# Kernel tuning notes

Hardware: AMD Instinct MI355X
Metric: run time of the kernel (lower is better)

## Reference

```python
import jax, jax.numpy as jnp
import numpy as np

DIM = 32
ED = DIM * DIM          # 1024
HID = ED * 4            # 4096
EPS = 1e-5


def _ln(x, g, b):
    # LayerNorm over last two dims (d, d)
    m = x.mean(axis=(-2, -1), keepdims=True)
    v = jnp.var(x, axis=(-2, -1), keepdims=True)
    return (x - m) * jax.lax.rsqrt(v + EPS) * g + b


def setup_inputs() -> dict:
    key = jax.random.key(0)
    ks = jax.random.split(key, 10)
    b, s, d = 2, 1024, DIM
    inp = {
        "x": jax.random.normal(ks[0], (b, s, d, d), dtype=jnp.float32),
        # StateSpaceLayer params
        "log_A": jax.random.normal(ks[1], (d,), dtype=jnp.float32) * 0.02,
        "w_dt": jax.random.normal(ks[2], (d,), dtype=jnp.float32) / np.sqrt(d),
        "b_dt": jnp.zeros((), dtype=jnp.float32),
        "g_ssm": jnp.ones((d, d), dtype=jnp.float32),
        "b_ssm": jnp.zeros((d, d), dtype=jnp.float32),
        # FFN params
        "g_ffn": jnp.ones((d, d), dtype=jnp.float32),
        "b_ffn": jnp.zeros((d, d), dtype=jnp.float32),
        "W1": jax.random.normal(ks[3], (ED, HID), dtype=jnp.float32) / np.sqrt(ED),
        "bb1": jnp.zeros((HID,), dtype=jnp.float32),
        "W2": jax.random.normal(ks[4], (HID, ED), dtype=jnp.float32) / np.sqrt(HID),
        "bb2": jnp.zeros((ED,), dtype=jnp.float32),
    }
    return inp


def reference(x, log_A, w_dt, b_dt, g_ssm, b_ssm, g_ffn, b_ffn, W1, bb1, W2, bb2):
    b, s, d, _ = x.shape
    # ---- StateSpaceLayer (parallel / training path) ----
    xn = _ln(x, g_ssm, b_ssm)                          # (b,s,d,d)
    A_cont = -jnp.exp(log_A)                           # (d,)
    # dt_proj: Linear(d,1) over last axis, then squeeze -> (b,s,d)
    dt = jax.nn.softplus(jnp.einsum('bsrc,c->bsr', xn, w_dt) + b_dt)
    log_a = dt * A_cont                                # (b,s,d)
    cs = jnp.cumsum(log_a, axis=1)                     # (b,s,d)
    log_M = cs[:, :, None, :] - cs[:, None, :, :]      # (b,t,j,d)
    tmask = jnp.arange(s)[:, None] >= jnp.arange(s)[None, :]  # (t,j) causal
    M = jnp.where(tmask[None, :, :, None], jnp.exp(log_M), 0.0)
    ssm_out = jnp.einsum('btjr,bjrc->btrc', M, xn) + x  # residual
    # ---- MatrixFeedForward ----
    fn = _ln(ssm_out, g_ffn, b_ffn).reshape(b, s, d * d)
    h = jax.nn.gelu(fn @ W1 + bb1, approximate=False)
    y = (h @ W2 + bb2).reshape(b, s, d, d)
    return ssm_out + y
```

## Files before the change

### kernel.cpp

```cpp
#include <hip/hip_runtime.h>
#include <math.h>

#define EPSF 1e-5f

typedef __attribute__((ext_vector_type(4))) float f32x4;
typedef __attribute__((ext_vector_type(2))) long long2v;

__device__ __forceinline__ unsigned short f2bf(float f) {
  unsigned int u = __float_as_uint(f);
  u += 0x7FFFu + ((u >> 16) & 1u);
  return (unsigned short)(u >> 16);
}
__device__ __forceinline__ float bf2f(unsigned short u) {
  return __uint_as_float((unsigned int)u << 16);
}


__global__ __launch_bounds__(256) void k_pre(
    const float* __restrict__ x, const float* __restrict__ g, const float* __restrict__ bta,
    const float* __restrict__ w_dt, const float* __restrict__ b_dt,
    const float* __restrict__ log_A, unsigned short* __restrict__ xn, float* __restrict__ log_a,
    const float* __restrict__ W1, unsigned char* __restrict__ W1t,
    const float* __restrict__ W2, unsigned char* __restrict__ W2t) {
  __shared__ float smem[64 * 65];
  int tid = threadIdx.x;
  if (blockIdx.x < 2048) {
    int bs = blockIdx.x;
    int t = tid;
    float4 v = ((const float4*)(x + (size_t)bs * 1024))[t];
    float s = v.x + v.y + v.z + v.w;
    float ss = v.x * v.x + v.y * v.y + v.z * v.z + v.w * v.w;
    #pragma unroll
    for (int o = 1; o < 64; o <<= 1) { s += __shfl_xor(s, o); ss += __shfl_xor(ss, o); }
    float* red = smem;
    int w = t >> 6;
    if ((t & 63) == 0) { red[w] = s; red[4 + w] = ss; }
    __syncthreads();
    float S = red[0] + red[1] + red[2] + red[3];
    float SS = red[4] + red[5] + red[6] + red[7];
    float m = S * (1.0f / 1024.0f);
    float var = SS * (1.0f / 1024.0f) - m * m;
    float inv = rsqrtf(var + EPSF);
    float4 gv = ((const float4*)g)[t];
    float4 bv = ((const float4*)bta)[t];
    float4 o;
    o.x = (v.x - m) * inv * gv.x + bv.x;
    o.y = (v.y - m) * inv * gv.y + bv.y;
    o.z = (v.z - m) * inv * gv.z + bv.z;
    o.w = (v.w - m) * inv * gv.w + bv.w;
    ushort4 ob;
    ob.x = f2bf(o.x); ob.y = f2bf(o.y); ob.z = f2bf(o.z); ob.w = f2bf(o.w);
    ((ushort4*)(xn + (size_t)bs * 1024))[t] = ob;
    float4 wv = ((const float4*)w_dt)[t & 7];
    float part = o.x * wv.x + o.y * wv.y + o.z * wv.z + o.w * wv.w;
    part += __shfl_xor(part, 1);
    part += __shfl_xor(part, 2);
    part += __shfl_xor(part, 4);
    if ((t & 7) == 0) {
      int r = t >> 3;
      float z = part + b_dt[0];
      float sp = (z > 20.0f) ? z : log1pf(expf(z));
      log_a[(size_t)bs * 32 + r] = sp * (-expf(log_A[r]));
    }
  } else {
    int bid = blockIdx.x - 2048;
    bool isW1 = bid < 1024;
    const float* src; unsigned char* dst; int C, r0, c0, nkgp;
    if (isW1) { src = W1; dst = W1t; C = 4096; nkgp = 16;
                c0 = (bid & 63) * 64; r0 = (bid >> 6) * 64; }
    else { bid -= 1024; src = W2; dst = W2t; C = 1024; nkgp = 64;
           c0 = (bid & 15) * 64; r0 = (bid >> 4) * 64; }
    #pragma unroll
    for (int q = 0; q < 4; ++q) {
      int lin = q * 256 + tid;
      int r = lin >> 4, cq = lin & 15;
      float4 v = *(const float4*)(src + (size_t)(r0 + r) * C + c0 + cq * 4);
      smem[r * 65 + cq * 4 + 0] = v.x; smem[r * 65 + cq * 4 + 1] = v.y;
      smem[r * 65 + cq * 4 + 2] = v.z; smem[r * 65 + cq * 4 + 3] = v.w;
    }
    __syncthreads();
    #pragma unroll
    for (int q = 0; q < 2; ++q) {
      int lin = q * 256 + tid;
      int c = lin & 63, rh = lin >> 6;
      int n = c0 + c, k = r0 + rh * 8;
      int nt = n >> 4, l15n = n & 15;
      int kp = k >> 6, qd = (k >> 3) & 3, half = (k >> 5) & 1;
      int p0 = __builtin_amdgcn_cvt_pk_fp8_f32(
          smem[(rh * 8 + 0) * 65 + c] * 16.0f, smem[(rh * 8 + 1) * 65 + c] * 16.0f, 0, false);
      p0 = __builtin_amdgcn_cvt_pk_fp8_f32(
          smem[(rh * 8 + 2) * 65 + c] * 16.0f, smem[(rh * 8 + 3) * 65 + c] * 16.0f, p0, true);
      int p1 = __builtin_amdgcn_cvt_pk_fp8_f32(
          smem[(rh * 8 + 4) * 65 + c] * 16.0f, smem[(rh * 8 + 5) * 65 + c] * 16.0f, 0, false);
      p1 = __builtin_amdgcn_cvt_pk_fp8_f32(
          smem[(rh * 8 + 6) * 65 + c] * 16.0f, smem[(rh * 8 + 7) * 65 + c] * 16.0f, p1, true);
      int2 pk; pk.x = p0; pk.y = p1;
      *(int2*)(dst + ((size_t)(nt * nkgp + kp)) * 1024 + (qd * 16 + l15n) * 16 + half * 8) = pk;
    }
  }
}

template <int PASS>
__global__ __launch_bounds__(256) void k_scan_pass(
    const unsigned short* __restrict__ xn, const float* __restrict__ x,
    const float* __restrict__ loga, float4* __restrict__ E, float* __restrict__ P,
    const float* __restrict__ bb2, float* __restrict__ out) {
  int bx = blockIdx.x;
  int b = bx >> 8, r = (bx >> 3) & 31, ch = bx & 7;
  int tid = threadIdx.x, cg = tid & 7, sub = tid >> 3;
  __shared__ float dec[128];
  __shared__ float4 sE[32][8];
  __shared__ float sP[32];
  if (tid < 128)
    dec[tid] = expf(loga[(size_t)(b * 1024 + ch * 128 + tid) * 32 + r]);
  __syncthreads();
  int t0 = ch * 128 + sub * 4;
  size_t base = ((size_t)(b * 1024 + t0) * 1024 + r * 32 + cg * 4) >> 2;
  const ushort4* xn4 = (const ushort4*)xn;
  float4 xv[4];
  #pragma unroll
  for (int i = 0; i < 4; ++i) {
    ushort4 u = xn4[base + (size_t)i * 256];
    xv[i].x = bf2f(u.x); xv[i].y = bf2f(u.y); xv[i].z = bf2f(u.z); xv[i].w = bf2f(u.w);
  }
  float4 S = {0.f, 0.f, 0.f, 0.f};
  float Pl = 1.0f;
  #pragma unroll
  for (int i = 0; i < 4; ++i) {
    float d = dec[sub * 4 + i];
    S.x = d * S.x + xv[i].x; S.y = d * S.y + xv[i].y;
    S.z = d * S.z + xv[i].z; S.w = d * S.w + xv[i].w;
    Pl *= d;
  }
  sE[sub][cg] = S;
  if (cg == 0) sP[sub] = Pl;
  __syncthreads();
  if (PASS == 0) {
    if (tid < 8) {
      float4 Et = {0.f, 0.f, 0.f, 0.f};
      float PP = 1.0f;
      #pragma unroll
      for (int h = 0; h < 32; ++h) {
        float p = sP[h]; float4 e = sE[h][tid];
        Et.x = p * Et.x + e.x; Et.y = p * Et.y + e.y;
        Et.z = p * Et.z + e.z; Et.w = p * Et.w + e.w;
        PP *= p;
      }
      E[((size_t)(b * 32 + r) * 8 + ch) * 8 + tid] = Et;
      if (tid == 0) P[(b * 32 + r) * 8 + ch] = PP;
    }
  } else {
    float4 Sin = {0.f, 0.f, 0.f, 0.f};
    const float4* Eb = E + (size_t)(b * 32 + r) * 64 + cg;
    const float* Pb = P + (size_t)(b * 32 + r) * 8;
    for (int h = 0; h < ch; ++h) {
      float p = Pb[h]; float4 e = Eb[h * 8];
      Sin.x = p * Sin.x + e.x; Sin.y = p * Sin.y + e.y;
      Sin.z = p * Sin.z + e.z; Sin.w = p * Sin.w + e.w;
    }
    for (int h = 0; h < sub; ++h) {
      float p = sP[h]; float4 e = sE[h][cg];
      Sin.x = p * Sin.x + e.x; Sin.y = p * Sin.y + e.y;
      Sin.z = p * Sin.z + e.z; Sin.w = p * Sin.w + e.w;
    }
    float4 bb = ((const float4*)bb2)[r * 8 + cg];
    const float4* x4 = (const float4*)x;
    float4* out4 = (float4*)out;
    #pragma unroll
    for (int i = 0; i < 4; ++i) {
      float d = dec[sub * 4 + i];
      Sin.x = d * Sin.x + xv[i].x; Sin.y = d * Sin.y + xv[i].y;
      Sin.z = d * Sin.z + xv[i].z; Sin.w = d * Sin.w + xv[i].w;
      float4 rx = x4[base + (size_t)i * 256];
      float4 oi;
      oi.x = Sin.x + rx.x + bb.x; oi.y = Sin.y + rx.y + bb.y;
      oi.z = Sin.z + rx.z + bb.z; oi.w = Sin.w + rx.w + bb.w;
      out4[base + (size_t)i * 256] = oi;
    }
  }
}

__global__ __launch_bounds__(256) void k_ln2(
    const float* __restrict__ out, const float* __restrict__ bb2,
    const float* __restrict__ g, const float* __restrict__ bta,
    unsigned char* __restrict__ fn) {
  int bs = blockIdx.x;
  int t = threadIdx.x;
  float4 v = ((const float4*)(out + (size_t)bs * 1024))[t];
  float4 bb = ((const float4*)bb2)[t];
  v.x -= bb.x; v.y -= bb.y; v.z -= bb.z; v.w -= bb.w;
  float s = v.x + v.y + v.z + v.w;
  float ss = v.x * v.x + v.y * v.y + v.z * v.z + v.w * v.w;
  #pragma unroll
  for (int o = 1; o < 64; o <<= 1) { s += __shfl_xor(s, o); ss += __shfl_xor(ss, o); }
  __shared__ float red[8];
  int w = t >> 6;
  if ((t & 63) == 0) { red[w] = s; red[4 + w] = ss; }
  __syncthreads();
  float S = red[0] + red[1] + red[2] + red[3];
  float SS = red[4] + red[5] + red[6] + red[7];
  float m = S * (1.0f / 1024.0f);
  float var = SS * (1.0f / 1024.0f) - m * m;
  float inv = rsqrtf(var + EPSF);
  float4 gv = ((const float4*)g)[t];
  float4 bv = ((const float4*)bta)[t];
  float f0 = (v.x - m) * inv * gv.x + bv.x;
  float f1 = (v.y - m) * inv * gv.y + bv.y;
  float f2 = (v.z - m) * inv * gv.z + bv.z;
  float f3 = (v.w - m) * inv * gv.w + bv.w;
  int p = __builtin_amdgcn_cvt_pk_fp8_f32(f0, f1, 0, false);
  p = __builtin_amdgcn_cvt_pk_fp8_f32(f2, f3, p, true);
  int mt = bs >> 4, l15m = bs & 15;
  int kp = t >> 4, qd = (t >> 1) & 3, half = (t >> 3) & 1, j0 = (t & 1) * 4;
  *(int*)(fn + ((size_t)(mt * 16 + kp)) * 1024 + (qd * 16 + l15m) * 16 + half * 8 + j0) = p;
}

__global__ __launch_bounds__(256, 2) void k_gemm1(
    const unsigned char* __restrict__ Ap, const unsigned char* __restrict__ Bp,
    const float* __restrict__ bias, unsigned char* __restrict__ C8) {
  constexpr int NKGP = 16, ITERP = 16;
  __shared__ __align__(16) unsigned char sC[16384];
  int L = blockIdx.x;
  int xcd = L & 7;
  int nq = xcd & 3, mh = xcd >> 2;
  int rest = L >> 3;
  int nx = rest & 7, my = rest >> 3;
  int n0 = (nq * 8 + nx) * 128;
  int m0 = (mh * 8 + my) * 128;
  int tid = threadIdx.x;
  int wave = tid >> 6, lane = tid & 63;
  int wr = wave >> 1, wc = wave & 1;
  int l15 = lane & 15, quad = lane >> 4;
  int mt0 = (m0 >> 4) + wr * 4;
  int nt0 = (n0 >> 4) + wc * 4;
  const unsigned char* pa = Ap + (size_t)mt0 * NKGP * 1024 + lane * 16;
  const unsigned char* pb = Bp + (size_t)nt0 * NKGP * 1024 + lane * 16;

  f32x4 zero = {0.0f, 0.0f, 0.0f, 0.0f};
  f32x4 acc[4][4];
  #pragma unroll
  for (int i = 0; i < 4; ++i)
    #pragma unroll
    for (int j = 0; j < 4; ++j) acc[i][j] = zero;

  long2v a[4][4], b[4][4];
  #pragma unroll
  for (int s = 0; s < 4; ++s)
    #pragma unroll
    for (int i = 0; i < 4; ++i) {
      a[s][i] = *(const long2v*)(pa + ((size_t)i * NKGP + s) * 1024);
      b[s][i] = *(const long2v*)(pb + ((size_t)i * NKGP + s) * 1024);
    }
  #pragma unroll 1
  for (int kp = 0; kp < ITERP - 4; kp += 4) {
    #pragma unroll
    for (int s = 0; s < 4; ++s) {
      #pragma unroll
      for (int i = 0; i < 4; ++i)
        #pragma unroll
        for (int j = 0; j < 4; ++j)
          acc[i][j] = __builtin_amdgcn_mfma_f32_16x16x32_fp8_fp8(a[s][i].x, b[s][j].x, acc[i][j], 0, 0, 0);
      #pragma unroll
      for (int i = 0; i < 4; ++i)
        #pragma unroll
        for (int j = 0; j < 4; ++j)
          acc[i][j] = __builtin_amdgcn_mfma_f32_16x16x32_fp8_fp8(a[s][i].y, b[s][j].y, acc[i][j], 0, 0, 0);
      #pragma unroll
      for (int i = 0; i < 4; ++i) {
        a[s][i] = *(const long2v*)(pa + ((size_t)i * NKGP + kp + 4 + s) * 1024);
        b[s][i] = *(const long2v*)(pb + ((size_t)i * NKGP + kp + 4 + s) * 1024);
      }
    }
  }
  #pragma unroll
  for (int s = 0; s < 4; ++s) {
    #pragma unroll
    for (int i = 0; i < 4; ++i)
      #pragma unroll
      for (int j = 0; j < 4; ++j)
        acc[i][j] = __builtin_amdgcn_mfma_f32_16x16x32_fp8_fp8(a[s][i].x, b[s][j].x, acc[i][j], 0, 0, 0);
    #pragma unroll
    for (int i = 0; i < 4; ++i)
      #pragma unroll
      for (int j = 0; j < 4; ++j)
        acc[i][j] = __builtin_amdgcn_mfma_f32_16x16x32_fp8_fp8(a[s][i].y, b[s][j].y, acc[i][j], 0, 0, 0);
  }

  #pragma unroll
  for (int i = 0; i < 4; ++i) {
    #pragma unroll
    for (int j = 0; j < 4; ++j) {
      int col_l = wc * 64 + j * 16 + l15;
      float bval = bias[n0 + col_l];
      int kp_l = col_l >> 6, q2 = (col_l >> 3) & 3, half2 = (col_l >> 5) & 1, j2 = col_l & 7;
      unsigned char* ldst = sC + ((wr * 4 + i) * 2 + kp_l) * 1024 + q2 * 256 + half2 * 8 + j2;
      float vv[4];
      #pragma unroll
      for (int v = 0; v < 4; ++v) {
        float val = acc[i][j][v] * 0.0625f + bval;
        vv[v] = 0.5f * val * (1.0f + erff(val * 0.70710678118654752f));
      }
      int p01 = __builtin_amdgcn_cvt_pk_fp8_f32(vv[0], vv[1], 0, false);
      int p23 = __builtin_amdgcn_cvt_pk_fp8_f32(vv[2], vv[3], 0, false);
      ldst[(quad * 4 + 0) * 16] = (unsigned char)(p01 & 0xff);
      ldst[(quad * 4 + 1) * 16] = (unsigned char)((p01 >> 8) & 0xff);
      ldst[(quad * 4 + 2) * 16] = (unsigned char)(p23 & 0xff);
      ldst[(quad * 4 + 3) * 16] = (unsigned char)((p23 >> 8) & 0xff);
    }
  }
  __syncthreads();
  int mt2_0 = m0 >> 4, kp2_0 = n0 >> 6;
  #pragma unroll
  for (int p = 0; p < 4; ++p) {
    int ci = p * 256 + tid;
    int sb = ci >> 6, off = (ci & 63) * 16;
    int mt2 = mt2_0 + (sb >> 1), kp2 = kp2_0 + (sb & 1);
    *(int4*)(C8 + ((size_t)(mt2 * 64 + kp2)) * 1024 + off) =
        *(const int4*)(sC + sb * 1024 + off);
  }
}

__global__ __launch_bounds__(256, 2) void k_gemm2(
    const unsigned char* __restrict__ Ap, const unsigned char* __restrict__ Bp,
    float* __restrict__ O) {
  constexpr int NKGP = 64, ITERP = 16;
  int L = blockIdx.x;
  int xcd = L & 7;
  int ks = xcd >> 1, mh = xcd & 1;
  int rest = L >> 3;
  int nx = rest & 7, my = rest >> 3;
  int n0 = nx * 128;
  int m0 = (mh * 8 + my) * 128;
  int kp0 = ks * ITERP;
  int tid = threadIdx.x;
  int wave = tid >> 6, lane = tid & 63;
  int wr = wave >> 1, wc = wave & 1;
  int l15 = lane & 15, quad = lane >> 4;
  int mt0 = (m0 >> 4) + wr * 4;
  int nt0 = (n0 >> 4) + wc * 4;
  const unsigned char* pa = Ap + ((size_t)mt0 * NKGP + kp0) * 1024 + lane * 16;
  const unsigned char* pb = Bp + ((size_t)nt0 * NKGP + kp0) * 1024 + lane * 16;

  f32x4 zero = {0.0f, 0.0f, 0.0f, 0.0f};
  f32x4 acc[4][4];
  #pragma unroll
  for (int i = 0; i < 4; ++i)
    #pragma unroll
    for (int j = 0; j < 4; ++j) acc[i][j] = zero;

  long2v a[4][4], b[4][4];
  #pragma unroll
  for (int s = 0; s < 4; ++s)
    #pragma unroll
    for (int i = 0; i < 4; ++i) {
      a[s][i] = *(const long2v*)(pa + ((size_t)i * NKGP + s) * 1024);
      b[s][i] = *(const long2v*)(pb + ((size_t)i * NKGP + s) * 1024);
    }
  #pragma unroll 1
  for (int kp = 0; kp < ITERP - 4; kp += 4) {
    #pragma unroll
    for (int s = 0; s < 4; ++s) {
      #pragma unroll
      for (int i = 0; i < 4; ++i)
        #pragma unroll
        for (int j = 0; j < 4; ++j)
          acc[i][j] = __builtin_amdgcn_mfma_f32_16x16x32_fp8_fp8(a[s][i].x, b[s][j].x, acc[i][j], 0, 0, 0);
      #pragma unroll
      for (int i = 0; i < 4; ++i)
        #pragma unroll
        for (int j = 0; j < 4; ++j)
          acc[i][j] = __builtin_amdgcn_mfma_f32_16x16x32_fp8_fp8(a[s][i].y, b[s][j].y, acc[i][j], 0, 0, 0);
      #pragma unroll
      for (int i = 0; i < 4; ++i) {
        a[s][i] = *(const long2v*)(pa + ((size_t)i * NKGP + kp + 4 + s) * 1024);
        b[s][i] = *(const long2v*)(pb + ((size_t)i * NKGP + kp + 4 + s) * 1024);
      }
    }
  }
  #pragma unroll
  for (int s = 0; s < 4; ++s) {
    #pragma unroll
    for (int i = 0; i < 4; ++i)
      #pragma unroll
      for (int j = 0; j < 4; ++j)
        acc[i][j] = __builtin_amdgcn_mfma_f32_16x16x32_fp8_fp8(a[s][i].x, b[s][j].x, acc[i][j], 0, 0, 0);
    #pragma unroll
    for (int i = 0; i < 4; ++i)
      #pragma unroll
      for (int j = 0; j < 4; ++j)
        acc[i][j] = __builtin_amdgcn_mfma_f32_16x16x32_fp8_fp8(a[s][i].y, b[s][j].y, acc[i][j], 0, 0, 0);
  }

  #pragma unroll
  for (int i = 0; i < 4; ++i)
    #pragma unroll
    for (int j = 0; j < 4; ++j) {
      int col = n0 + wc * 64 + j * 16 + l15;
      #pragma unroll
      for (int v = 0; v < 4; ++v) {
        int row = m0 + wr * 64 + i * 16 + quad * 4 + v;
        atomicAdd(&O[(size_t)row * 1024 + col], acc[i][j][v] * 0.0625f);
      }
    }
}

extern "C" void kernel_launch(void* const* d_in, const int* in_sizes, int n_in,
                              void* d_out, int out_size, void* d_ws, size_t ws_size,
                              hipStream_t stream) {
  const float* x     = (const float*)d_in[0];
  const float* log_A = (const float*)d_in[1];
  const float* w_dt  = (const float*)d_in[2];
  const float* b_dt  = (const float*)d_in[3];
  const float* g_ssm = (const float*)d_in[4];
  const float* b_ssm = (const float*)d_in[5];
  const float* g_ffn = (const float*)d_in[6];
  const float* b_ffn = (const float*)d_in[7];
  const float* W1    = (const float*)d_in[8];
  const float* bb1   = (const float*)d_in[9];
  const float* W2    = (const float*)d_in[10];
  const float* bb2   = (const float*)d_in[11];
  float* out = (float*)d_out;

  const size_t MB = 1u << 20;
  char* ws = (char*)d_ws;
  unsigned short* xn   = (unsigned short*)(ws);
  unsigned char* W1t   = (unsigned char*)(ws + 4 * MB);
  float* loga          = (float*)(ws + 8 * MB);
  float4* Ebuf         = (float4*)(ws + 8 * MB + 262144);
  float* Pbuf          = (float*)(ws + 8 * MB + 393216);
  unsigned char* fn    = (unsigned char*)(ws + 9 * MB);
  unsigned char* W2t   = (unsigned char*)(ws + 11 * MB);
  unsigned char* hbf   = (unsigned char*)(ws + 15 * MB);

  k_pre<<<4096, 256, 0, stream>>>(x, g_ssm, b_ssm, w_dt, b_dt, log_A, xn, loga,
                                  W1, W1t, W2, W2t);
  k_scan_pass<0><<<512, 256, 0, stream>>>(xn, x, loga, Ebuf, Pbuf, bb2, out);
  k_scan_pass<1><<<512, 256, 0, stream>>>(xn, x, loga, Ebuf, Pbuf, bb2, out);
  k_ln2<<<2048, 256, 0, stream>>>(out, bb2, g_ffn, b_ffn, fn);
  k_gemm1<<<512, 256, 0, stream>>>(fn, W1t, bb1, hbf);
  k_gemm2<<<512, 256, 0, stream>>>(hbf, W2t, out);
}
```

Before: 174.6 us.

## Stage GEMM operand tiles in LDS via async global-to-LDS loads

The two FP8 GEMM kernels are merged into one template that stages A and B tiles in a 64KB shared buffer. Each wave issues global_load_lds copies for its share of the tiles, and every wave then reads its fragments from LDS. Before, each wave fetched its own fragments straight from global memory into registers. The goal is to share operand loads across waves and cut redundant global traffic and register pressure. In exchange the pipeline is single-buffered, with two barriers per stage and no overlap of load and compute, and 64KB of LDS per block may limit occupancy.

After: 173.9 us. No clear change (-0.4%).

```diff
diff --git a/kernel.cpp b/kernel.cpp
--- a/kernel.cpp
+++ b/kernel.cpp
@@ -13,6 +13,12 @@
 }
 __device__ __forceinline__ float bf2f(unsigned short u) {
   return __uint_as_float((unsigned int)u << 16);
+}
+
+__device__ __forceinline__ void async_load16(const void* g, void* l) {
+  __builtin_amdgcn_global_load_lds(
+      (const __attribute__((address_space(1))) void*)g,
+      (__attribute__((address_space(3))) void*)l, 16, 0, 0);
 }
 
 
@@ -215,26 +221,37 @@
   *(int*)(fn + ((size_t)(mt * 16 + kp)) * 1024 + (qd * 16 + l15m) * 16 + half * 8 + j0) = p;
 }
 
-__global__ __launch_bounds__(256, 2) void k_gemm1(
+template <int EPI, int NKGP>
+__global__ __launch_bounds__(256, 2) void k_gemm_lds(
     const unsigned char* __restrict__ Ap, const unsigned char* __restrict__ Bp,
-    const float* __restrict__ bias, unsigned char* __restrict__ C8) {
-  constexpr int NKGP = 16, ITERP = 16;
-  __shared__ __align__(16) unsigned char sC[16384];
+    const float* __restrict__ bias, void* __restrict__ C) {
+  __shared__ __align__(16) unsigned char sAB[65536];
+  unsigned char* sA = sAB;
+  unsigned char* sB = sAB + 32768;
   int L = blockIdx.x;
-  int xcd = L & 7;
-  int nq = xcd & 3, mh = xcd >> 2;
-  int rest = L >> 3;
-  int nx = rest & 7, my = rest >> 3;
-  int n0 = (nq * 8 + nx) * 128;
-  int m0 = (mh * 8 + my) * 128;
+  int m0, n0, kp0;
+  if (EPI == 0) {
+    int xcd = L & 7;
+    int nq = xcd & 3, mh = xcd >> 2;
+    int rest = L >> 3;
+    int nx = rest & 7, my = rest >> 3;
+    n0 = (nq * 8 + nx) * 128;
+    m0 = (mh * 8 + my) * 128;
+    kp0 = 0;
+  } else {
+    int xcd = L & 7;
+    int ks = xcd >> 1, mh = xcd & 1;
+    int rest = L >> 3;
+    int nx = rest & 7, my = rest >> 3;
+    n0 = nx * 128;
+    m0 = (mh * 8 + my) * 128;
+    kp0 = ks * 16;
+  }
   int tid = threadIdx.x;
   int wave = tid >> 6, lane = tid & 63;
   int wr = wave >> 1, wc = wave & 1;
   int l15 = lane & 15, quad = lane >> 4;
-  int mt0 = (m0 >> 4) + wr * 4;
-  int nt0 = (n0 >> 4) + wc * 4;
-  const unsigned char* pa = Ap + (size_t)mt0 * NKGP * 1024 + lane * 16;
-  const unsigned char* pb = Bp + (size_t)nt0 * NKGP * 1024 + lane * 16;
+  int mt0b = m0 >> 4, nt0b = n0 >> 4;
 
   f32x4 zero = {0.0f, 0.0f, 0.0f, 0.0f};
   f32x4 acc[4][4];
@@ -243,165 +260,94 @@
     #pragma unroll
     for (int j = 0; j < 4; ++j) acc[i][j] = zero;
 
-  long2v a[4][4], b[4][4];
-  #pragma unroll
-  for (int s = 0; s < 4; ++s)
-    #pragma unroll
-    for (int i = 0; i < 4; ++i) {
-      a[s][i] = *(const long2v*)(pa + ((size_t)i * NKGP + s) * 1024);
-      b[s][i] = *(const long2v*)(pb + ((size_t)i * NKGP + s) * 1024);
-    }
+  const unsigned char* gsrc = (wave < 2) ? Ap : Bp;
+  int rt0 = (wave < 2) ? mt0b : nt0b;
+  unsigned char* ldst = ((wave < 2) ? sA : sB) + (wave & 1) * 16384;
+  int sb0 = (wave & 1) * 16;
+
   #pragma unroll 1
-  for (int kp = 0; kp < ITERP - 4; kp += 4) {
-    #pragma unroll
-    for (int s = 0; s < 4; ++s) {
+  for (int st = 0; st < 4; ++st) {
+    int kps = kp0 + st * 4;
+    #pragma unroll
+    for (int t = 0; t < 16; ++t) {
+      int sb = sb0 + t;
+      int rt = sb >> 2, kl = sb & 3;
+      async_load16(gsrc + ((size_t)(rt0 + rt) * NKGP + kps + kl) * 1024 + lane * 16,
+                   ldst + t * 1024);
+    }
+    __syncthreads();
+    #pragma unroll
+    for (int kl = 0; kl < 4; ++kl) {
+      long2v af[4], bf[4];
+      #pragma unroll
+      for (int i = 0; i < 4; ++i)
+        af[i] = *(const long2v*)(sA + ((wr * 4 + i) * 4 + kl) * 1024 + lane * 16);
+      #pragma unroll
+      for (int j = 0; j < 4; ++j)
+        bf[j] = *(const long2v*)(sB + ((wc * 4 + j) * 4 + kl) * 1024 + lane * 16);
       #pragma unroll
       for (int i = 0; i < 4; ++i)
         #pragma unroll
         for (int j = 0; j < 4; ++j)
-          acc[i][j] = __builtin_amdgcn_mfma_f32_16x16x32_fp8_fp8(a[s][i].x, b[s][j].x, acc[i][j], 0, 0, 0);
+          acc[i][j] = __builtin_amdgcn_mfma_f32_16x16x32_fp8_fp8(af[i].x, bf[j].x, acc[i][j], 0, 0, 0);
       #pragma unroll
       for (int i = 0; i < 4; ++i)
         #pragma unroll
         for (int j = 0; j < 4; ++j)
-          acc[i][j] = __builtin_amdgcn_mfma_f32_16x16x32_fp8_fp8(a[s][i].y, b[s][j].y, acc[i][j], 0, 0, 0);
-      #pragma unroll
-      for (int i = 0; i < 4; ++i) {
-        a[s][i] = *(const long2v*)(pa + ((size_t)i * NKGP + kp + 4 + s) * 1024);
-        b[s][i] = *(const long2v*)(pb + ((size_t)i * NKGP + kp + 4 + s) * 1024);
+          acc[i][j] = __builtin_amdgcn_mfma_f32_16x16x32_fp8_fp8(af[i].y, bf[j].y, acc[i][j], 0, 0, 0);
+    }
+    __syncthreads();
+  }
+
+  if (EPI == 0) {
+    unsigned char* sC = sAB;
+    #pragma unroll
+    for (int i = 0; i < 4; ++i) {
+      #pragma unroll
+      for (int j = 0; j < 4; ++j) {
+        int col_l = wc * 64 + j * 16 + l15;
+        float bval = bias[n0 + col_l];
+        int kp_l = col_l >> 6, q2 = (col_l >> 3) & 3, half2 = (col_l >> 5) & 1, j2 = col_l & 7;
+        unsigned char* ld = sC + ((wr * 4 + i) * 2 + kp_l) * 1024 + q2 * 256 + half2 * 8 + j2;
+        float vv[4];
+        #pragma unroll
+        for (int v = 0; v < 4; ++v) {
+          float val = acc[i][j][v] * 0.0625f + bval;
+          vv[v] = 0.5f * val * (1.0f + erff(val * 0.70710678118654752f));
+        }
+        int p01 = __builtin_amdgcn_cvt_pk_fp8_f32(vv[0], vv[1], 0, false);
+        int p23 = __builtin_amdgcn_cvt_pk_fp8_f32(vv[2], vv[3], 0, false);
+        ld[(quad * 4 + 0) * 16] = (unsigned char)(p01 & 0xff);
+        ld[(quad * 4 + 1) * 16] = (unsigned char)((p01 >> 8) & 0xff);
+        ld[(quad * 4 + 2) * 16] = (unsigned char)(p23 & 0xff);
+        ld[(quad * 4 + 3) * 16] = (unsigned char)((p23 >> 8) & 0xff);
       }
     }
-  }
-  #pragma unroll
-  for (int s = 0; s < 4; ++s) {
+    __syncthreads();
+    unsigned char* C8 = (unsigned char*)C;
+    int mt2_0 = m0 >> 4, kp2_0 = n0 >> 6;
+    #pragma unroll
+    for (int p = 0; p < 4; ++p) {
+      int ci = p * 256 + tid;
+      int sb = ci >> 6, off = (ci & 63) * 16;
+      int mt2 = mt2_0 + (sb >> 1), kp2 = kp2_0 + (sb & 1);
+      *(int4*)(C8 + ((size_t)(mt2 * 64 + kp2)) * 1024 + off) =
+          *(const int4*)(sC + sb * 1024 + off);
+    }
+  } else {
+    float* O = (float*)C;
     #pragma unroll
     for (int i = 0; i < 4; ++i)
       #pragma unroll
-      for (int j = 0; j < 4; ++j)
-        acc[i][j] = __builtin_amdgcn_mfma_f32_16x16x32_fp8_fp8(a[s][i].x, b[s][j].x, acc[i][j], 0, 0, 0);
-    #pragma unroll
-    for (int i = 0; i < 4; ++i)
-      #pragma unroll
-      for (int j = 0; j < 4; ++j)
-        acc[i][j] = __builtin_amdgcn_mfma_f32_16x16x32_fp8_fp8(a[s][i].y, b[s][j].y, acc[i][j], 0, 0, 0);
-  }
-
-  #pragma unroll
-  for (int i = 0; i < 4; ++i) {
-    #pragma unroll
-    for (int j = 0; j < 4; ++j) {
-      int col_l = wc * 64 + j * 16 + l15;
-      float bval = bias[n0 + col_l];
-      int kp_l = col_l >> 6, q2 = (col_l >> 3) & 3, half2 = (col_l >> 5) & 1, j2 = col_l & 7;
-      unsigned char* ldst = sC + ((wr * 4 + i) * 2 + kp_l) * 1024 + q2 * 256 + half2 * 8 + j2;
-      float vv[4];
-      #pragma unroll
-      for (int v = 0; v < 4; ++v) {
-        float val = acc[i][j][v] * 0.0625f + bval;
-        vv[v] = 0.5f * val * (1.0f + erff(val * 0.70710678118654752f));
+      for (int j = 0; j < 4; ++j) {
+        int col = n0 + wc * 64 + j * 16 + l15;
+        #pragma unroll
+        for (int v = 0; v < 4; ++v) {
+          int row = m0 + wr * 64 + i * 16 + quad * 4 + v;
+          atomicAdd(&O[(size_t)row * 1024 + col], acc[i][j][v] * 0.0625f);
+        }
       }
-      int p01 = __builtin_amdgcn_cvt_pk_fp8_f32(vv[0], vv[1], 0, false);
-      int p23 = __builtin_amdgcn_cvt_pk_fp8_f32(vv[2], vv[3], 0, false);
-      ldst[(quad * 4 + 0) * 16] = (unsigned char)(p01 & 0xff);
-      ldst[(quad * 4 + 1) * 16] = (unsigned char)((p01 >> 8) & 0xff);
-      ldst[(quad * 4 + 2) * 16] = (unsigned char)(p23 & 0xff);
-      ldst[(quad * 4 + 3) * 16] = (unsigned char)((p23 >> 8) & 0xff);
-    }
-  }
-  __syncthreads();
-  int mt2_0 = m0 >> 4, kp2_0 = n0 >> 6;
-  #pragma unroll
-  for (int p = 0; p < 4; ++p) {
-    int ci = p * 256 + tid;
-    int sb = ci >> 6, off = (ci & 63) * 16;
-    int mt2 = mt2_0 + (sb >> 1), kp2 = kp2_0 + (sb & 1);
-    *(int4*)(C8 + ((size_t)(mt2 * 64 + kp2)) * 1024 + off) =
-        *(const int4*)(sC + sb * 1024 + off);
-  }
-}
-
-__global__ __launch_bounds__(256, 2) void k_gemm2(
-    const unsigned char* __restrict__ Ap, const unsigned char* __restrict__ Bp,
-    float* __restrict__ O) {
-  constexpr int NKGP = 64, ITERP = 16;
-  int L = blockIdx.x;
-  int xcd = L & 7;
-  int ks = xcd >> 1, mh = xcd & 1;
-  int rest = L >> 3;
-  int nx = rest & 7, my = rest >> 3;
-  int n0 = nx * 128;
-  int m0 = (mh * 8 + my) * 128;
-  int kp0 = ks * ITERP;
-  int tid = threadIdx.x;
-  int wave = tid >> 6, lane = tid & 63;
-  int wr = wave >> 1, wc = wave & 1;
-  int l15 = lane & 15, quad = lane >> 4;
-  int mt0 = (m0 >> 4) + wr * 4;
-  int nt0 = (n0 >> 4) + wc * 4;
-  const unsigned char* pa = Ap + ((size_t)mt0 * NKGP + kp0) * 1024 + lane * 16;
-  const unsigned char* pb = Bp + ((size_t)nt0 * NKGP + kp0) * 1024 + lane * 16;
-
-  f32x4 zero = {0.0f, 0.0f, 0.0f, 0.0f};
-  f32x4 acc[4][4];
-  #pragma unroll
-  for (int i = 0; i < 4; ++i)
-    #pragma unroll
-    for (int j = 0; j < 4; ++j) acc[i][j] = zero;
-
-  long2v a[4][4], b[4][4];
-  #pragma unroll
-  for (int s = 0; s < 4; ++s)
-    #pragma unroll
-    for (int i = 0; i < 4; ++i) {
-      a[s][i] = *(const long2v*)(pa + ((size_t)i * NKGP + s) * 1024);
-      b[s][i] = *(const long2v*)(pb + ((size_t)i * NKGP + s) * 1024);
-    }
-  #pragma unroll 1
-  for (int kp = 0; kp < ITERP - 4; kp += 4) {
-    #pragma unroll
-    for (int s = 0; s < 4; ++s) {
-      #pragma unroll
-      for (int i = 0; i < 4; ++i)
-        #pragma unroll
-        for (int j = 0; j < 4; ++j)
-          acc[i][j] = __builtin_amdgcn_mfma_f32_16x16x32_fp8_fp8(a[s][i].x, b[s][j].x, acc[i][j], 0, 0, 0);
-      #pragma unroll
-      for (int i = 0; i < 4; ++i)
-        #pragma unroll
-        for (int j = 0; j < 4; ++j)
-          acc[i][j] = __builtin_amdgcn_mfma_f32_16x16x32_fp8_fp8(a[s][i].y, b[s][j].y, acc[i][j], 0, 0, 0);
-      #pragma unroll
-      for (int i = 0; i < 4; ++i) {
-        a[s][i] = *(const long2v*)(pa + ((size_t)i * NKGP + kp + 4 + s) * 1024);
-        b[s][i] = *(const long2v*)(pb + ((size_t)i * NKGP + kp + 4 + s) * 1024);
-      }
-    }
-  }
-  #pragma unroll
-  for (int s = 0; s < 4; ++s) {
-    #pragma unroll
-    for (int i = 0; i < 4; ++i)
-      #pragma unroll
-      for (int j = 0; j < 4; ++j)
-        acc[i][j] = __builtin_amdgcn_mfma_f32_16x16x32_fp8_fp8(a[s][i].x, b[s][j].x, acc[i][j], 0, 0, 0);
-    #pragma unroll
-    for (int i = 0; i < 4; ++i)
-      #pragma unroll
-      for (int j = 0; j < 4; ++j)
-        acc[i][j] = __builtin_amdgcn_mfma_f32_16x16x32_fp8_fp8(a[s][i].y, b[s][j].y, acc[i][j], 0, 0, 0);
-  }
-
-  #pragma unroll
-  for (int i = 0; i < 4; ++i)
-    #pragma unroll
-    for (int j = 0; j < 4; ++j) {
-      int col = n0 + wc * 64 + j * 16 + l15;
-      #pragma unroll
-      for (int v = 0; v < 4; ++v) {
-        int row = m0 + wr * 64 + i * 16 + quad * 4 + v;
-        atomicAdd(&O[(size_t)row * 1024 + col], acc[i][j][v] * 0.0625f);
-      }
-    }
+  }
 }
 
 extern "C" void kernel_launch(void* const* d_in, const int* in_sizes, int n_in,
@@ -437,6 +383,6 @@
   k_scan_pass<0><<<512, 256, 0, stream>>>(xn, x, loga, Ebuf, Pbuf, bb2, out);
   k_scan_pass<1><<<512, 256, 0, stream>>>(xn, x, loga, Ebuf, Pbuf, bb2, out);
   k_ln2<<<2048, 256, 0, stream>>>(out, bb2, g_ffn, b_ffn, fn);
-  k_gemm1<<<512, 256, 0, stream>>>(fn, W1t, bb1, hbf);
-  k_gemm2<<<512, 256, 0, stream>>>(hbf, W2t, out);
-}
+  k_gemm_lds<0, 16><<<512, 256, 0, stream>>>(fn, W1t, bb1, (void*)hbf);
+  k_gemm_lds<1, 64><<<512, 256, 0, stream>>>(hbf, W2t, nullptr, (void*)out);
+}
```

## Fuse all phases into one cooperative persistent kernel with grid syncs

Applied to the files above, without the earlier changes.

Turns the six separate kernels into device phase functions and runs them in a single cooperative launch of 512 blocks, with grid-wide syncs and thread fences between phases. Each block loops over several units in the pre and LayerNorm phases. The aim is to remove the launch gaps and tail idle time between kernels. In exchange, grid syncs add barrier cost and the occupancy is fixed at two blocks per CU with a shared dynamic smem size. If the cooperative launch fails, the code falls back to the per-phase kernels.

After: 185.9 us. 6.5% more time.

```diff
diff --git a/kernel.cpp b/kernel.cpp
--- a/kernel.cpp
+++ b/kernel.cpp
@@ -1,7 +1,11 @@
 #include <hip/hip_runtime.h>
+#include <hip/hip_cooperative_groups.h>
 #include <math.h>
 
+namespace cg = cooperative_groups;
+
 #define EPSF 1e-5f
+#define SMEM_BYTES 16640
 
 typedef __attribute__((ext_vector_type(4))) float f32x4;
 typedef __attribute__((ext_vector_type(2))) long long2v;
@@ -16,16 +20,18 @@
 }
 
 
-__global__ __launch_bounds__(256) void k_pre(
+
+__device__ void phase_pre(int unit, char* smem_raw,
     const float* __restrict__ x, const float* __restrict__ g, const float* __restrict__ bta,
     const float* __restrict__ w_dt, const float* __restrict__ b_dt,
     const float* __restrict__ log_A, unsigned short* __restrict__ xn, float* __restrict__ log_a,
     const float* __restrict__ W1, unsigned char* __restrict__ W1t,
     const float* __restrict__ W2, unsigned char* __restrict__ W2t) {
-  __shared__ float smem[64 * 65];
+  float* smem = (float*)smem_raw;
   int tid = threadIdx.x;
-  if (blockIdx.x < 2048) {
-    int bs = blockIdx.x;
+  __syncthreads();
+  if (unit < 2048) {
+    int bs = unit;
     int t = tid;
     float4 v = ((const float4*)(x + (size_t)bs * 1024))[t];
     float s = v.x + v.y + v.z + v.w;
@@ -63,7 +69,7 @@
       log_a[(size_t)bs * 32 + r] = sp * (-expf(log_A[r]));
     }
   } else {
-    int bid = blockIdx.x - 2048;
+    int bid = unit - 2048;
     bool isW1 = bid < 1024;
     const float* src; unsigned char* dst; int C, r0, c0, nkgp;
     if (isW1) { src = W1; dst = W1t; C = 4096; nkgp = 16;
@@ -101,21 +107,21 @@
 }
 
 template <int PASS>
-__global__ __launch_bounds__(256) void k_scan_pass(
+__device__ void phase_scan(int bx, char* smem_raw,
     const unsigned short* __restrict__ xn, const float* __restrict__ x,
     const float* __restrict__ loga, float4* __restrict__ E, float* __restrict__ P,
     const float* __restrict__ bb2, float* __restrict__ out) {
-  int bx = blockIdx.x;
+  float4* sE = (float4*)smem_raw;
+  float* dec = (float*)(smem_raw + 4096);
+  float* sP  = (float*)(smem_raw + 4608);
   int b = bx >> 8, r = (bx >> 3) & 31, ch = bx & 7;
-  int tid = threadIdx.x, cg = tid & 7, sub = tid >> 3;
-  __shared__ float dec[128];
-  __shared__ float4 sE[32][8];
-  __shared__ float sP[32];
+  int tid = threadIdx.x, cg_ = tid & 7, sub = tid >> 3;
+  __syncthreads();
   if (tid < 128)
     dec[tid] = expf(loga[(size_t)(b * 1024 + ch * 128 + tid) * 32 + r]);
   __syncthreads();
   int t0 = ch * 128 + sub * 4;
-  size_t base = ((size_t)(b * 1024 + t0) * 1024 + r * 32 + cg * 4) >> 2;
+  size_t base = ((size_t)(b * 1024 + t0) * 1024 + r * 32 + cg_ * 4) >> 2;
   const ushort4* xn4 = (const ushort4*)xn;
   float4 xv[4];
   #pragma unroll
@@ -132,8 +138,8 @@
     S.z = d * S.z + xv[i].z; S.w = d * S.w + xv[i].w;
     Pl *= d;
   }
-  sE[sub][cg] = S;
-  if (cg == 0) sP[sub] = Pl;
+  sE[sub * 8 + cg_] = S;
+  if (cg_ == 0) sP[sub] = Pl;
   __syncthreads();
   if (PASS == 0) {
     if (tid < 8) {
@@ -141,7 +147,7 @@
       float PP = 1.0f;
       #pragma unroll
       for (int h = 0; h < 32; ++h) {
-        float p = sP[h]; float4 e = sE[h][tid];
+        float p = sP[h]; float4 e = sE[h * 8 + tid];
         Et.x = p * Et.x + e.x; Et.y = p * Et.y + e.y;
         Et.z = p * Et.z + e.z; Et.w = p * Et.w + e.w;
         PP *= p;
@@ -151,7 +157,7 @@
     }
   } else {
     float4 Sin = {0.f, 0.f, 0.f, 0.f};
-    const float4* Eb = E + (size_t)(b * 32 + r) * 64 + cg;
+    const float4* Eb = E + (size_t)(b * 32 + r) * 64 + cg_;
     const float* Pb = P + (size_t)(b * 32 + r) * 8;
     for (int h = 0; h < ch; ++h) {
       float p = Pb[h]; float4 e = Eb[h * 8];
@@ -159,11 +165,11 @@
       Sin.z = p * Sin.z + e.z; Sin.w = p * Sin.w + e.w;
     }
     for (int h = 0; h < sub; ++h) {
-      float p = sP[h]; float4 e = sE[h][cg];
+      float p = sP[h]; float4 e = sE[h * 8 + cg_];
       Sin.x = p * Sin.x + e.x; Sin.y = p * Sin.y + e.y;
       Sin.z = p * Sin.z + e.z; Sin.w = p * Sin.w + e.w;
     }
-    float4 bb = ((const float4*)bb2)[r * 8 + cg];
+    float4 bb = ((const float4*)bb2)[r * 8 + cg_];
     const float4* x4 = (const float4*)x;
     float4* out4 = (float4*)out;
     #pragma unroll
@@ -180,12 +186,13 @@
   }
 }
 
-__global__ __launch_bounds__(256) void k_ln2(
+__device__ void phase_ln2(int bs, char* smem_raw,
     const float* __restrict__ out, const float* __restrict__ bb2,
     const float* __restrict__ g, const float* __restrict__ bta,
     unsigned char* __restrict__ fn) {
-  int bs = blockIdx.x;
+  float* red = (float*)smem_raw;
   int t = threadIdx.x;
+  __syncthreads();
   float4 v = ((const float4*)(out + (size_t)bs * 1024))[t];
   float4 bb = ((const float4*)bb2)[t];
   v.x -= bb.x; v.y -= bb.y; v.z -= bb.z; v.w -= bb.w;
@@ -193,7 +200,6 @@
   float ss = v.x * v.x + v.y * v.y + v.z * v.z + v.w * v.w;
   #pragma unroll
   for (int o = 1; o < 64; o <<= 1) { s += __shfl_xor(s, o); ss += __shfl_xor(ss, o); }
-  __shared__ float red[8];
   int w = t >> 6;
   if ((t & 63) == 0) { red[w] = s; red[4 + w] = ss; }
   __syncthreads();
@@ -215,12 +221,11 @@
   *(int*)(fn + ((size_t)(mt * 16 + kp)) * 1024 + (qd * 16 + l15m) * 16 + half * 8 + j0) = p;
 }
 
-__global__ __launch_bounds__(256, 2) void k_gemm1(
+__device__ void phase_gemm1(int L, char* smem_raw,
     const unsigned char* __restrict__ Ap, const unsigned char* __restrict__ Bp,
     const float* __restrict__ bias, unsigned char* __restrict__ C8) {
   constexpr int NKGP = 16, ITERP = 16;
-  __shared__ __align__(16) unsigned char sC[16384];
-  int L = blockIdx.x;
+  unsigned char* sC = (unsigned char*)smem_raw;
   int xcd = L & 7;
   int nq = xcd & 3, mh = xcd >> 2;
   int rest = L >> 3;
@@ -286,6 +291,7 @@
         acc[i][j] = __builtin_amdgcn_mfma_f32_16x16x32_fp8_fp8(a[s][i].y, b[s][j].y, acc[i][j], 0, 0, 0);
   }
 
+  __syncthreads();
   #pragma unroll
   for (int i = 0; i < 4; ++i) {
     #pragma unroll
@@ -293,7 +299,7 @@
       int col_l = wc * 64 + j * 16 + l15;
       float bval = bias[n0 + col_l];
       int kp_l = col_l >> 6, q2 = (col_l >> 3) & 3, half2 = (col_l >> 5) & 1, j2 = col_l & 7;
-      unsigned char* ldst = sC + ((wr * 4 + i) * 2 + kp_l) * 1024 + q2 * 256 + half2 * 8 + j2;
+      unsigned char* ld = sC + ((wr * 4 + i) * 2 + kp_l) * 1024 + q2 * 256 + half2 * 8 + j2;
       float vv[4];
       #pragma unroll
       for (int v = 0; v < 4; ++v) {
@@ -302,10 +308,10 @@
       }
       int p01 = __builtin_amdgcn_cvt_pk_fp8_f32(vv[0], vv[1], 0, false);
       int p23 = __builtin_amdgcn_cvt_pk_fp8_f32(vv[2], vv[3], 0, false);
-      ldst[(quad * 4 + 0) * 16] = (unsigned char)(p01 & 0xff);
-      ldst[(quad * 4 + 1) * 16] = (unsigned char)((p01 >> 8) & 0xff);
-      ldst[(quad * 4 + 2) * 16] = (unsigned char)(p23 & 0xff);
-      ldst[(quad * 4 + 3) * 16] = (unsigned char)((p23 >> 8) & 0xff);
+      ld[(quad * 4 + 0) * 16] = (unsigned char)(p01 & 0xff);
+      ld[(quad * 4 + 1) * 16] = (unsigned char)((p01 >> 8) & 0xff);
+      ld[(quad * 4 + 2) * 16] = (unsigned char)(p23 & 0xff);
+      ld[(quad * 4 + 3) * 16] = (unsigned char)((p23 >> 8) & 0xff);
     }
   }
   __syncthreads();
@@ -320,11 +326,10 @@
   }
 }
 
-__global__ __launch_bounds__(256, 2) void k_gemm2(
+__device__ void phase_gemm2(int L,
     const unsigned char* __restrict__ Ap, const unsigned char* __restrict__ Bp,
     float* __restrict__ O) {
   constexpr int NKGP = 64, ITERP = 16;
-  int L = blockIdx.x;
   int xcd = L & 7;
   int ks = xcd >> 1, mh = xcd & 1;
   int rest = L >> 3;
@@ -402,6 +407,50 @@
         atomicAdd(&O[(size_t)row * 1024 + col], acc[i][j][v] * 0.0625f);
       }
     }
+}
+
+
+#define ALL_PARAMS \
+    const float* x, const float* log_A, const float* w_dt, const float* b_dt, \
+    const float* g_ssm, const float* b_ssm, const float* g_ffn, const float* b_ffn, \
+    const float* W1, const float* bb1, const float* W2, const float* bb2, \
+    float* out, unsigned short* xn, unsigned char* W1t, float* loga, \
+    float4* Ebuf, float* Pbuf, unsigned char* fn, unsigned char* W2t, unsigned char* hbf
+
+#define ALL_ARGS x, log_A, w_dt, b_dt, g_ssm, b_ssm, g_ffn, b_ffn, W1, bb1, W2, bb2, \
+    out, xn, W1t, loga, Ebuf, Pbuf, fn, W2t, hbf
+
+__global__ __launch_bounds__(256, 2) void k_mega(ALL_PARAMS) {
+  extern __shared__ char smem[];
+  cg::grid_group gg = cg::this_grid();
+  int bid = blockIdx.x;
+  #pragma unroll 1
+  for (int u = 0; u < 8; ++u)
+    phase_pre(bid * 8 + u, smem, x, g_ssm, b_ssm, w_dt, b_dt, log_A, xn, loga, W1, W1t, W2, W2t);
+  __threadfence(); gg.sync(); __threadfence();
+  phase_scan<0>(bid, smem, xn, x, loga, Ebuf, Pbuf, bb2, out);
+  __threadfence(); gg.sync(); __threadfence();
+  phase_scan<1>(bid, smem, xn, x, loga, Ebuf, Pbuf, bb2, out);
+  __threadfence(); gg.sync(); __threadfence();
+  #pragma unroll 1
+  for (int q = 0; q < 4; ++q)
+    phase_ln2(bid * 4 + q, smem, out, bb2, g_ffn, b_ffn, fn);
+  __threadfence(); gg.sync(); __threadfence();
+  phase_gemm1(bid, smem, fn, W1t, bb1, hbf);
+  __threadfence(); gg.sync(); __threadfence();
+  phase_gemm2(bid, hbf, W2t, out);
+}
+
+template <int P>
+__global__ __launch_bounds__(256, 2) void k_phase(ALL_PARAMS) {
+  extern __shared__ char smem[];
+  int bid = blockIdx.x;
+  if (P == 0) phase_pre(bid, smem, x, g_ssm, b_ssm, w_dt, b_dt, log_A, xn, loga, W1, W1t, W2, W2t);
+  if (P == 1) phase_scan<0>(bid, smem, xn, x, loga, Ebuf, Pbuf, bb2, out);
+  if (P == 2) phase_scan<1>(bid, smem, xn, x, loga, Ebuf, Pbuf, bb2, out);
+  if (P == 3) phase_ln2(bid, smem, out, bb2, g_ffn, b_ffn, fn);
+  if (P == 4) phase_gemm1(bid, smem, fn, W1t, bb1, hbf);
+  if (P == 5) phase_gemm2(bid, hbf, W2t, out);
 }
 
 extern "C" void kernel_launch(void* const* d_in, const int* in_sizes, int n_in,
@@ -432,11 +481,28 @@
   unsigned char* W2t   = (unsigned char*)(ws + 11 * MB);
   unsigned char* hbf   = (unsigned char*)(ws + 15 * MB);
 
-  k_pre<<<4096, 256, 0, stream>>>(x, g_ssm, b_ssm, w_dt, b_dt, log_A, xn, loga,
-                                  W1, W1t, W2, W2t);
-  k_scan_pass<0><<<512, 256, 0, stream>>>(xn, x, loga, Ebuf, Pbuf, bb2, out);
-  k_scan_pass<1><<<512, 256, 0, stream>>>(xn, x, loga, Ebuf, Pbuf, bb2, out);
-  k_ln2<<<2048, 256, 0, stream>>>(out, bb2, g_ffn, b_ffn, fn);
-  k_gemm1<<<512, 256, 0, stream>>>(fn, W1t, bb1, hbf);
-  k_gemm2<<<512, 256, 0, stream>>>(hbf, W2t, out);
-}
+  int dev = 0;
+  (void)hipGetDevice(&dev);
+  int coop = 0;
+  (void)hipDeviceGetAttribute(&coop, hipDeviceAttributeCooperativeLaunch, dev);
+  int nb = 0;
+  if (coop)
+    (void)hipOccupancyMaxActiveBlocksPerMultiprocessor(&nb, k_mega, 256, SMEM_BYTES);
+  if (coop && nb >= 2) {
+    void* args[] = {(void*)&x, (void*)&log_A, (void*)&w_dt, (void*)&b_dt,
+                    (void*)&g_ssm, (void*)&b_ssm, (void*)&g_ffn, (void*)&b_ffn,
+                    (void*)&W1, (void*)&bb1, (void*)&W2, (void*)&bb2,
+                    (void*)&out, (void*)&xn, (void*)&W1t, (void*)&loga,
+                    (void*)&Ebuf, (void*)&Pbuf, (void*)&fn, (void*)&W2t, (void*)&hbf};
+    hipError_t e = hipLaunchCooperativeKernel((const void*)k_mega, dim3(512), dim3(256),
+                                              args, SMEM_BYTES, stream);
+    if (e == hipSuccess) return;
+    (void)hipGetLastError();
+  }
+  k_phase<0><<<4096, 256, SMEM_BYTES, stream>>>(ALL_ARGS);
+  k_phase<1><<<512,  256, SMEM_BYTES, stream>>>(ALL_ARGS);
+  k_phase<2><<<512,  256, SMEM_BYTES, stream>>>(ALL_ARGS);
+  k_phase<3><<<2048, 256, SMEM_BYTES, stream>>>(ALL_ARGS);
+  k_phase<4><<<512,  256, SMEM_BYTES, stream>>>(ALL_ARGS);
+  k_phase<5><<<512,  256, SMEM_BYTES, stream>>>(ALL_ARGS);
+}
```
